# Kernel tuning notes

Measured on AMD Instinct MI355X. Metric: run time of the kernel, lower is better.

## Reference

```python
import jax, jax.numpy as jnp
import numpy as np
import math

WIN = 2
TOPK = 3
GH, GW = 4, 4  # gabor splatting grid == upsampled window size


def _window_partition(img, ws):
    # img: (B, C, H, W) -> (B, num_windows, ws*ws, C)
    B, C, H, W = img.shape
    x = img.transpose(0, 2, 3, 1)  # B,H,W,C
    x = x.reshape(B, H // ws, ws, W // ws, ws, C)
    x = x.transpose(0, 1, 3, 2, 4, 5).reshape(B, -1, ws * ws, C)
    return x


def _gabor_map(theta, sigma, lam, psi, gamma):
    # build num 4x4 Gabor kernels from per-component params -> (num, GH, GW)
    cy = jnp.arange(GH, dtype=jnp.float32) - (GH - 1) / 2.0
    cx = jnp.arange(GW, dtype=jnp.float32) - (GW - 1) / 2.0
    yy, xx = jnp.meshgrid(cy, cx, indexing='ij')  # (GH, GW)
    th = theta[:, None, None] * (2.0 * jnp.pi)
    xp = xx[None] * jnp.cos(th) + yy[None] * jnp.sin(th)
    yp = -xx[None] * jnp.sin(th) + yy[None] * jnp.cos(th)
    sig = sigma[:, None, None] + 0.5  # keep positive
    lmb = lam[:, None, None] + 0.5
    gam = gamma[:, None, None]
    env = jnp.exp(-(xp ** 2 + (gam ** 2) * yp ** 2) / (2.0 * sig ** 2))
    carrier = jnp.cos(2.0 * jnp.pi * xp / lmb + psi[:, None, None])
    return env * carrier  # (num, GH, GW)


def setup_inputs() -> dict:
    key = jax.random.key(0)
    ks = jax.random.split(key, 8)
    B, Nt, Ns, C = 64, 64, 4096, 256
    return {
        'z': jax.random.normal(ks[0], (B, Nt, C), dtype=jnp.float32),
        'x': jax.random.normal(ks[1], (B, Ns, C), dtype=jnp.float32),
        'gabor_theta': jax.random.uniform(ks[2], (16,), dtype=jnp.float32),
        'gabor_sigma': jax.random.uniform(ks[3], (16,), dtype=jnp.float32),
        'gabor_lam': jax.random.uniform(ks[4], (16,), dtype=jnp.float32),
        'gabor_psi': jax.random.uniform(ks[5], (16,), dtype=jnp.float32),
        'gabor_gamma': jax.random.uniform(ks[6], (16,), dtype=jnp.float32),
        'gabor_weight': jax.random.normal(ks[7], (16,), dtype=jnp.float32),
    }


def reference(z, x, gabor_theta, gabor_sigma, gabor_lam, gabor_psi,
              gabor_gamma, gabor_weight):
    B, Nt, C = z.shape
    ht = int(math.isqrt(Nt))
    _, Ns, _ = x.shape
    hs = int(math.isqrt(Ns))

    z_img = z.transpose(0, 2, 1).reshape(B, C, ht, ht)
    z_max = z_img.max(axis=(2, 3))  # AdaptiveMaxPool2d((1,1)) -> (B, C)

    x_img = x.transpose(0, 2, 1).reshape(B, C, hs, hs)
    x_windows = _window_partition(x_img, WIN)

    # grouped 1x1 xcorr == per-pixel dot product with template vector
    response = jnp.einsum('bchw,bc->bhw', x_img, z_max)[:, None]  # (B,1,hs,hs)
    r_windows = _window_partition(response, WIN)
    win_mean = r_windows.mean(axis=2)[..., 0]  # (B, nW)

    _, idx = jax.lax.top_k(win_mean, TOPK)  # (B, TOPK)
    x_sel = jnp.take_along_axis(x_windows, idx[:, :, None, None], axis=1)
    x_win = x_sel.reshape(B, TOPK, WIN, WIN, C).transpose(0, 1, 4, 2, 3)
    x_win = x_win.reshape(B * TOPK, C, WIN, WIN)

    x_up = jax.image.resize(x_win, (B * TOPK, C, GH, GW), method='bilinear')

    g = _gabor_map(gabor_theta, gabor_sigma, gabor_lam, gabor_psi, gabor_gamma)
    gmap = jnp.einsum('k,khw->hw', gabor_weight, g)  # (GH, GW)
    splat = x_up * gmap  # gabor splatting as multiplicative spatial modulation

    res = (splat + x_up).reshape(B, TOPK, C, GH * GW)
    res = res.transpose(0, 1, 3, 2).reshape(B, TOPK * GH * GW, C)
    return res
```

## Files before the change

### kernel.cpp

```cpp
#include <hip/hip_runtime.h>
#include <math.h>

#define TWO_PI 6.28318530717958647692f


__global__ void k_zmax(const float* __restrict__ z, float* __restrict__ zmax) {
    int b = blockIdx.x;
    int c = threadIdx.x;
    const float* zp = z + (size_t)b * 64 * 256 + c;
    float m = -INFINITY;
#pragma unroll
    for (int n = 0; n < 64; ++n) m = fmaxf(m, zp[n * 256]);
    zmax[b * 256 + c] = m;
}

__global__ void k_wmean(const float* __restrict__ x, const float* __restrict__ zmax,
                        float* __restrict__ wmean) {
    int blk  = blockIdx.x;
    int b    = blk >> 5;
    int wh   = blk & 31;
    int wave = threadIdx.x >> 6;
    int lane = threadIdx.x & 63;
    int g    = lane >> 4;
    int q    = lane & 15;

    const float4* zm4 = (const float4*)(zmax + b * 256);
    float4 zm0 = zm4[q];
    float4 zm1 = zm4[q + 16];
    float4 zm2 = zm4[q + 32];
    float4 zm3 = zm4[q + 48];

    const float4* xb = (const float4*)(x + (size_t)b * 4096 * 256);
    int trow = (2 * wh + (g >> 1)) * 64;
    float* wout = wmean + b * 1024 + wh * 32;

#pragma unroll
    for (int p = 0; p < 8; ++p) {
        int ww  = p * 4 + wave;
        int tok = trow + 2 * ww + (g & 1);
        const float4* tp = xb + (size_t)tok * 64;
        float4 v0 = tp[q];
        float4 v1 = tp[q + 16];
        float4 v2 = tp[q + 32];
        float4 v3 = tp[q + 48];
        float d = v0.x * zm0.x + v0.y * zm0.y + v0.z * zm0.z + v0.w * zm0.w
                + v1.x * zm1.x + v1.y * zm1.y + v1.z * zm1.z + v1.w * zm1.w
                + v2.x * zm2.x + v2.y * zm2.y + v2.z * zm2.z + v2.w * zm2.w
                + v3.x * zm3.x + v3.y * zm3.y + v3.z * zm3.z + v3.w * zm3.w;
        d += __shfl_xor(d, 1, 64);
        d += __shfl_xor(d, 2, 64);
        d += __shfl_xor(d, 4, 64);
        d += __shfl_xor(d, 8, 64);
        d += __shfl_xor(d, 16, 64);
        d += __shfl_xor(d, 32, 64);
        if (lane == 0) wout[ww] = d * 0.25f;
    }
}

__global__ void k_topk(const float* __restrict__ wmean_g, int* __restrict__ idxout) {
    __shared__ float wmean[1024];
    __shared__ float rv[256];
    __shared__ int   ri[256];
    int b   = blockIdx.x;
    int tid = threadIdx.x;
    for (int widx = tid; widx < 1024; widx += 256) wmean[widx] = wmean_g[b * 1024 + widx];
    __syncthreads();
    for (int k = 0; k < 3; ++k) {
        float bv = -INFINITY;
        int   bi = 1 << 30;
        for (int widx = tid; widx < 1024; widx += 256) {
            float v = wmean[widx];
            if (v > bv || (v == bv && widx < bi)) { bv = v; bi = widx; }
        }
        rv[tid] = bv; ri[tid] = bi;
        __syncthreads();
        for (int s = 128; s > 0; s >>= 1) {
            if (tid < s) {
                float v2 = rv[tid + s]; int i2 = ri[tid + s];
                if (v2 > rv[tid] || (v2 == rv[tid] && i2 < ri[tid])) { rv[tid] = v2; ri[tid] = i2; }
            }
            __syncthreads();
        }
        if (tid == 0) {
            idxout[b * 3 + k] = ri[0];
            wmean[ri[0]] = -INFINITY;
        }
        __syncthreads();
    }
}

__global__ void k_out(const float* __restrict__ x, const int* __restrict__ idxbuf,
                      const float* __restrict__ theta, const float* __restrict__ sigma,
                      const float* __restrict__ lam,   const float* __restrict__ psi,
                      const float* __restrict__ gamma, const float* __restrict__ wgt,
                      float* __restrict__ out) {
    __shared__ float Xs[4 * 256];
    __shared__ float gm[16];
    int b = blockIdx.x / 3;
    int k = blockIdx.x % 3;
    int tid  = threadIdx.x;
    int tok  = tid >> 6;
    int lane = tid & 63;

    int widx = idxbuf[b * 3 + k];
    int h0 = (widx >> 5) << 1;
    int w0 = (widx & 31) << 1;
    int token_id = (h0 + (tok >> 1)) * 64 + w0 + (tok & 1);
    float4 v = ((const float4*)(x + ((size_t)b * 4096 + token_id) * 256))[lane];
    ((float4*)Xs)[tok * 64 + lane] = v;

    if (tid < 16) {
        int p = tid;
        float yy = (float)(p >> 2) - 1.5f;
        float xx = (float)(p & 3) - 1.5f;
        float acc = 0.0f;
        for (int kk = 0; kk < 16; ++kk) {
            float th = theta[kk] * TWO_PI;
            float sn, cs;
            sincosf(th, &sn, &cs);
            float xp = xx * cs + yy * sn;
            float yp = -xx * sn + yy * cs;
            float sig = sigma[kk] + 0.5f;
            float lmb = lam[kk] + 0.5f;
            float gam = gamma[kk];
            float env = expf(-(xp * xp + gam * gam * yp * yp) / (2.0f * sig * sig));
            float car = cosf(TWO_PI * xp / lmb + psi[kk]);
            acc += wgt[kk] * env * car;
        }
        gm[p] = 1.0f + acc;
    }
    __syncthreads();

    const float WT[4] = {1.0f, 0.75f, 0.25f, 0.0f};
    float4 x00 = ((const float4*)Xs)[0 * 64 + lane];
    float4 x01 = ((const float4*)Xs)[1 * 64 + lane];
    float4 x10 = ((const float4*)Xs)[2 * 64 + lane];
    float4 x11 = ((const float4*)Xs)[3 * 64 + lane];
    float4* ob = (float4*)(out + ((size_t)b * 48 + k * 16) * 256);
#pragma unroll
    for (int it = 0; it < 4; ++it) {
        int p  = it * 4 + (tid >> 6);
        int gy = p >> 2, gx = p & 3;
        float wy0 = WT[gy], wy1 = 1.0f - wy0;
        float wx0 = WT[gx], wx1 = 1.0f - wx0;
        float g = gm[p];
        float4 r;
        r.x = g * (wy0 * (wx0 * x00.x + wx1 * x01.x) + wy1 * (wx0 * x10.x + wx1 * x11.x));
        r.y = g * (wy0 * (wx0 * x00.y + wx1 * x01.y) + wy1 * (wx0 * x10.y + wx1 * x11.y));
        r.z = g * (wy0 * (wx0 * x00.z + wx1 * x01.z) + wy1 * (wx0 * x10.z + wx1 * x11.z));
        r.w = g * (wy0 * (wx0 * x00.w + wx1 * x01.w) + wy1 * (wx0 * x10.w + wx1 * x11.w));
        ob[(size_t)p * 64 + lane] = r;
    }
}

extern "C" void kernel_launch(void* const* d_in, const int* in_sizes, int n_in,
                              void* d_out, int out_size, void* d_ws, size_t ws_size,
                              hipStream_t stream) {
    const float* z     = (const float*)d_in[0];
    const float* x     = (const float*)d_in[1];
    const float* theta = (const float*)d_in[2];
    const float* sigma = (const float*)d_in[3];
    const float* lam   = (const float*)d_in[4];
    const float* psi   = (const float*)d_in[5];
    const float* gamma = (const float*)d_in[6];
    const float* wgt   = (const float*)d_in[7];
    float* out = (float*)d_out;

    float* ws    = (float*)d_ws;
    float* zmax  = ws;
    float* wmean = ws + 16384;
    int*   idxb  = (int*)(ws + 16384 + 65536);

    k_zmax<<<64, 256, 0, stream>>>(z, zmax);
    k_wmean<<<2048, 256, 0, stream>>>(x, zmax, wmean);
    k_topk<<<64, 256, 0, stream>>>(wmean, idxb);
    k_out<<<192, 256, 0, stream>>>(x, idxb, theta, sigma, lam, psi, gamma, wgt, out);
}
```

Measured before the change: 384.0 us.

## Fuse top-k selection into output kernel and use nontemporal loads for x

Removes the separate top-k kernel: each output block (b,k) redundantly repeats the top-k selection up to its own k from the window means, then gathers its window. It also switches the x reads in the window-mean kernel to nontemporal vector loads to reduce cache pollution while streaming the large input. This saves one launch and one global round trip at the cost of redundant selection work and a longer serial prefix in the output blocks.

New measurement: 361.3 us. 5.9% less time.

```diff
diff --git a/kernel.cpp b/kernel.cpp
--- a/kernel.cpp
+++ b/kernel.cpp
@@ -2,6 +2,8 @@
 #include <math.h>
 
 #define TWO_PI 6.28318530717958647692f
+
+typedef float vfloat4 __attribute__((ext_vector_type(4)));
 
 
 __global__ void k_zmax(const float* __restrict__ z, float* __restrict__ zmax) {
@@ -24,13 +26,13 @@
     int g    = lane >> 4;
     int q    = lane & 15;
 
-    const float4* zm4 = (const float4*)(zmax + b * 256);
-    float4 zm0 = zm4[q];
-    float4 zm1 = zm4[q + 16];
-    float4 zm2 = zm4[q + 32];
-    float4 zm3 = zm4[q + 48];
+    const vfloat4* zm4 = (const vfloat4*)(zmax + b * 256);
+    vfloat4 zm0 = zm4[q];
+    vfloat4 zm1 = zm4[q + 16];
+    vfloat4 zm2 = zm4[q + 32];
+    vfloat4 zm3 = zm4[q + 48];
 
-    const float4* xb = (const float4*)(x + (size_t)b * 4096 * 256);
+    const vfloat4* xb = (const vfloat4*)(x + (size_t)b * 4096 * 256);
     int trow = (2 * wh + (g >> 1)) * 64;
     float* wout = wmean + b * 1024 + wh * 32;
 
@@ -38,11 +40,11 @@
     for (int p = 0; p < 8; ++p) {
         int ww  = p * 4 + wave;
         int tok = trow + 2 * ww + (g & 1);
-        const float4* tp = xb + (size_t)tok * 64;
-        float4 v0 = tp[q];
-        float4 v1 = tp[q + 16];
-        float4 v2 = tp[q + 32];
-        float4 v3 = tp[q + 48];
+        const vfloat4* tp = xb + (size_t)tok * 64;
+        vfloat4 v0 = __builtin_nontemporal_load(tp + q);
+        vfloat4 v1 = __builtin_nontemporal_load(tp + q + 16);
+        vfloat4 v2 = __builtin_nontemporal_load(tp + q + 32);
+        vfloat4 v3 = __builtin_nontemporal_load(tp + q + 48);
         float d = v0.x * zm0.x + v0.y * zm0.y + v0.z * zm0.z + v0.w * zm0.w
                 + v1.x * zm1.x + v1.y * zm1.y + v1.z * zm1.z + v1.w * zm1.w
                 + v2.x * zm2.x + v2.y * zm2.y + v2.z * zm2.z + v2.w * zm2.w
@@ -57,57 +59,23 @@
     }
 }
 
-__global__ void k_topk(const float* __restrict__ wmean_g, int* __restrict__ idxout) {
-    __shared__ float wmean[1024];
-    __shared__ float rv[256];
-    __shared__ int   ri[256];
-    int b   = blockIdx.x;
-    int tid = threadIdx.x;
-    for (int widx = tid; widx < 1024; widx += 256) wmean[widx] = wmean_g[b * 1024 + widx];
-    __syncthreads();
-    for (int k = 0; k < 3; ++k) {
-        float bv = -INFINITY;
-        int   bi = 1 << 30;
-        for (int widx = tid; widx < 1024; widx += 256) {
-            float v = wmean[widx];
-            if (v > bv || (v == bv && widx < bi)) { bv = v; bi = widx; }
-        }
-        rv[tid] = bv; ri[tid] = bi;
-        __syncthreads();
-        for (int s = 128; s > 0; s >>= 1) {
-            if (tid < s) {
-                float v2 = rv[tid + s]; int i2 = ri[tid + s];
-                if (v2 > rv[tid] || (v2 == rv[tid] && i2 < ri[tid])) { rv[tid] = v2; ri[tid] = i2; }
-            }
-            __syncthreads();
-        }
-        if (tid == 0) {
-            idxout[b * 3 + k] = ri[0];
-            wmean[ri[0]] = -INFINITY;
-        }
-        __syncthreads();
-    }
-}
-
-__global__ void k_out(const float* __restrict__ x, const int* __restrict__ idxbuf,
+__global__ void k_out(const float* __restrict__ x, const float* __restrict__ wmean_g,
                       const float* __restrict__ theta, const float* __restrict__ sigma,
                       const float* __restrict__ lam,   const float* __restrict__ psi,
                       const float* __restrict__ gamma, const float* __restrict__ wgt,
                       float* __restrict__ out) {
+    __shared__ float wmean[1024];
+    __shared__ float rv[256];
+    __shared__ int   ri[256];
     __shared__ float Xs[4 * 256];
     __shared__ float gm[16];
+    __shared__ int   widx_s;
+
     int b = blockIdx.x / 3;
     int k = blockIdx.x % 3;
     int tid  = threadIdx.x;
     int tok  = tid >> 6;
     int lane = tid & 63;
-
-    int widx = idxbuf[b * 3 + k];
-    int h0 = (widx >> 5) << 1;
-    int w0 = (widx & 31) << 1;
-    int token_id = (h0 + (tok >> 1)) * 64 + w0 + (tok & 1);
-    float4 v = ((const float4*)(x + ((size_t)b * 4096 + token_id) * 256))[lane];
-    ((float4*)Xs)[tok * 64 + lane] = v;
 
     if (tid < 16) {
         int p = tid;
@@ -129,6 +97,39 @@
         }
         gm[p] = 1.0f + acc;
     }
+
+    for (int w = tid; w < 1024; w += 256) wmean[w] = wmean_g[b * 1024 + w];
+    __syncthreads();
+
+    for (int kk = 0; kk <= k; ++kk) {
+        float bv = -INFINITY;
+        int   bi = 1 << 30;
+        for (int w = tid; w < 1024; w += 256) {
+            float v = wmean[w];
+            if (v > bv || (v == bv && w < bi)) { bv = v; bi = w; }
+        }
+        rv[tid] = bv; ri[tid] = bi;
+        __syncthreads();
+        for (int s = 128; s > 0; s >>= 1) {
+            if (tid < s) {
+                float v2 = rv[tid + s]; int i2 = ri[tid + s];
+                if (v2 > rv[tid] || (v2 == rv[tid] && i2 < ri[tid])) { rv[tid] = v2; ri[tid] = i2; }
+            }
+            __syncthreads();
+        }
+        if (tid == 0) {
+            widx_s = ri[0];
+            wmean[ri[0]] = -INFINITY;
+        }
+        __syncthreads();
+    }
+
+    int widx = widx_s;
+    int h0 = (widx >> 5) << 1;
+    int w0 = (widx & 31) << 1;
+    int token_id = (h0 + (tok >> 1)) * 64 + w0 + (tok & 1);
+    float4 v = ((const float4*)(x + ((size_t)b * 4096 + token_id) * 256))[lane];
+    ((float4*)Xs)[tok * 64 + lane] = v;
     __syncthreads();
 
     const float WT[4] = {1.0f, 0.75f, 0.25f, 0.0f};
@@ -169,10 +170,8 @@
     float* ws    = (float*)d_ws;
     float* zmax  = ws;
     float* wmean = ws + 16384;
-    int*   idxb  = (int*)(ws + 16384 + 65536);
 
     k_zmax<<<64, 256, 0, stream>>>(z, zmax);
     k_wmean<<<2048, 256, 0, stream>>>(x, zmax, wmean);
-    k_topk<<<64, 256, 0, stream>>>(wmean, idxb);
-    k_out<<<192, 256, 0, stream>>>(x, idxb, theta, sigma, lam, psi, gamma, wgt, out);
+    k_out<<<192, 256, 0, stream>>>(x, wmean, theta, sigma, lam, psi, gamma, wgt, out);
 }
```
